# Performance work log

Measured on AMD Instinct MI355X. Metric: run time of the kernel, lower is better.

Reference implementation:

```python
import jax, jax.numpy as jnp
import numpy as np
from jax import lax

T = 0.2  # temperature

def _l2norm(x, axis):
    n = jnp.sqrt(jnp.sum(x * x, axis=axis, keepdims=True))
    return x / jnp.maximum(n, 1e-12)

def setup_inputs() -> dict:
    key = jax.random.key(0)
    k1, k2, k3, k4 = jax.random.split(key, 4)
    B, K, C, H, W, Q = 16, 5, 256, 128, 128, 64
    res1 = jax.random.normal(k1, (B, K, H, W), jnp.float32)
    fea1 = jax.random.normal(k2, (B, C, H, W), jnp.float32)
    gt = jax.random.randint(k3, (B, H, W), 0, K, dtype=jnp.int32)
    # queue buffers, L2-normalized along feature dim (torch normalize(dim=0) on [C,Q])
    queues = _l2norm(jax.random.normal(k4, (K, C, Q), jnp.float32), axis=1)
    return {"res1": res1, "fea1": fea1, "queues": queues, "gt": gt, "label_bs": 8}

def reference(res1, fea1, queues, gt, label_bs):
    B, K, H, W = res1.shape
    C = fea1.shape[1]
    HW = H * W
    # per-sample prediction: gt for labeled samples, argmax of logits otherwise
    pred_arg = jnp.argmax(res1, axis=1).reshape(B, HW)
    pred_gt = gt.reshape(B, HW).astype(pred_arg.dtype)
    labeled = (jnp.arange(B) < label_bs)[:, None]
    pred = jnp.where(labeled, pred_gt, pred_arg)  # [B, HW]

    fea = fea1.reshape(B, C, HW)
    # masked segment-mean per class (vectorized version of the per-unique-label loop)
    onehot = (pred[:, None, :] == jnp.arange(K)[None, :, None]).astype(fea.dtype)  # [B,K,HW]
    counts = onehot.sum(-1)                                    # [B,K]
    sums = jnp.einsum('bkp,bcp->bkc', onehot, fea)             # [B,K,C]
    means = sums / jnp.maximum(counts, 1.0)[..., None]
    keys_all = _l2norm(means, axis=-1)                         # [B,K,C]

    present = counts > 0                                       # [B,K]
    # Faithful replication of the source's off-by-one: keys[list(vals).index(c)]
    # selects the mean of the PREVIOUS present class (vals excludes the smallest
    # present label while keys keeps all unique labels in sorted order).
    idx = jnp.where(present, jnp.arange(K)[None, :], -1)
    cmax = lax.cummax(idx, axis=1)
    prev = jnp.concatenate([jnp.full((B, 1), -1, cmax.dtype), cmax[:, :-1]], axis=1)  # [B,K]
    smallest = jnp.argmax(present, axis=1)                     # first present class
    valid = present & (jnp.arange(K)[None, :] != smallest[:, None]) & (prev >= 0)

    query = jnp.take_along_axis(keys_all, jnp.maximum(prev, 0)[:, :, None], axis=1)  # [B,K,C]

    qd = lax.stop_gradient(queues)  # queues are detached buffers in the original
    sim = jnp.einsum('bkc,jcq->bkjq', query, qd) / T           # [B,K,K,Q]
    l_pos = jnp.einsum('bkc,kcq->bkq', query, qd) / T          # [B,K,Q]
    sumE = jnp.exp(sim).sum(-1)                                # [B,K,K]
    off = 1.0 - jnp.eye(K, dtype=sumE.dtype)
    neg = (sumE * off[None]).sum(-1)                           # [B,K] cross-class negatives
    l_neg = jnp.exp(l_pos) + neg[:, :, None]                   # [B,K,Q]
    log_prob = (l_pos - jnp.log(l_neg)).mean(-1)               # [B,K]

    loss_c = jnp.where(valid, -log_prob, 0.0)
    n_present = present.sum(1)
    denom = n_present - 1  # len(vals)
    per_sample = jnp.where(denom > 0, loss_c.sum(1) / jnp.maximum(denom, 1), 0.0)
    return per_sample.sum() / B
```

## Files before the change

### kernel.cpp

```cpp
#include <hip/hip_runtime.h>
#include <cstddef>

constexpr int B_  = 16;
constexpr int K_  = 5;
constexpr int C_  = 256;
constexpr int HW_ = 128 * 128;
constexpr int Q_  = 64;
constexpr float T_ = 0.2f;

typedef float f4 __attribute__((ext_vector_type(4)));

__global__ __launch_bounds__(256) void pred_kernel(
    const float* __restrict__ res1, const int* __restrict__ gt,
    const int* __restrict__ label_bs, unsigned int* __restrict__ predp,
    int* __restrict__ counts_i)
{
    int idx = blockIdx.x * 256 + threadIdx.x;
    int b  = idx >> 12;
    int p4 = idx & 4095;
    int lb = label_bs[0];
    int k0, k1, k2, k3;
    if (b < lb) {
        int4 g = reinterpret_cast<const int4*>(gt + (size_t)b * HW_)[p4];
        k0 = g.x; k1 = g.y; k2 = g.z; k3 = g.w;
    } else {
        const float4* r = reinterpret_cast<const float4*>(res1 + (size_t)b * K_ * HW_) + p4;
        float4 best = r[0];
        k0 = k1 = k2 = k3 = 0;
        #pragma unroll
        for (int k = 1; k < K_; ++k) {
            float4 v = r[(size_t)k * (HW_ / 4)];
            if (v.x > best.x) { best.x = v.x; k0 = k; }
            if (v.y > best.y) { best.y = v.y; k1 = k; }
            if (v.z > best.z) { best.z = v.z; k2 = k; }
            if (v.w > best.w) { best.w = v.w; k3 = k; }
        }
    }
    predp[idx] = (unsigned)k0 | ((unsigned)k1 << 8) | ((unsigned)k2 << 16) | ((unsigned)k3 << 24);

    int cnt[K_];
    #pragma unroll
    for (int k = 0; k < K_; ++k)
        cnt[k] = (k0 == k) + (k1 == k) + (k2 == k) + (k3 == k);

    int lane = threadIdx.x & 63, wv = threadIdx.x >> 6;
    __shared__ int redc[4][K_];
    #pragma unroll
    for (int k = 0; k < K_; ++k) {
        int v = cnt[k];
        #pragma unroll
        for (int off = 32; off > 0; off >>= 1) v += __shfl_down(v, off);
        if (lane == 0) redc[wv][k] = v;
    }
    __syncthreads();
    if (threadIdx.x < K_)
        atomicAdd(&counts_i[b * K_ + threadIdx.x],
                  redc[0][threadIdx.x] + redc[1][threadIdx.x] +
                  redc[2][threadIdx.x] + redc[3][threadIdx.x]);
}

__global__ __launch_bounds__(256) void segsum_kernel(
    const float* __restrict__ fea, const unsigned int* __restrict__ predp,
    float* __restrict__ sums)
{
    int tid = threadIdx.x;
    int lane = tid & 63, wv = tid >> 6;
    __shared__ float red[4][K_];

    #pragma unroll
    for (int r = 0; r < 2; ++r) {
        int bc = blockIdx.x + r * 2048;
        int b = bc >> 8;
        int c = bc & (C_ - 1);
        const f4* frow = reinterpret_cast<const f4*>(fea + ((size_t)b * C_ + c) * HW_);
        const unsigned int* prow = predp + (size_t)b * (HW_ / 4);

        float acc[K_] = {};
        #pragma unroll 4
        for (int i = tid; i < HW_ / 4; i += 256) {
            f4 v = __builtin_nontemporal_load(frow + i);
            unsigned u = prow[i];
            int k0 = u & 255, k1 = (u >> 8) & 255, k2 = (u >> 16) & 255, k3 = u >> 24;
            #pragma unroll
            for (int k = 0; k < K_; ++k) {
                acc[k] += (k0 == k ? v.x : 0.f)
                        + (k1 == k ? v.y : 0.f)
                        + (k2 == k ? v.z : 0.f)
                        + (k3 == k ? v.w : 0.f);
            }
        }

        #pragma unroll
        for (int k = 0; k < K_; ++k) {
            float v = acc[k];
            #pragma unroll
            for (int off = 32; off > 0; off >>= 1) v += __shfl_down(v, off);
            if (lane == 0) red[wv][k] = v;
        }
        __syncthreads();
        if (tid < K_)
            sums[((size_t)b * K_ + tid) * C_ + c] =
                red[0][tid] + red[1][tid] + red[2][tid] + red[3][tid];
        __syncthreads();
    }
}

__global__ __launch_bounds__(256) void loss_kernel(
    const float* __restrict__ sums, const int* __restrict__ counts_i,
    const float* __restrict__ queues, float* __restrict__ logprob,
    int* __restrict__ flag, float* __restrict__ out)
{
    int bk = blockIdx.x;
    int b = bk / K_;
    int k = bk - b * K_;
    int tid = threadIdx.x, lane = tid & 63, wv = tid >> 6;

    __shared__ float key[C_];
    __shared__ float wred[4];
    __shared__ float sumE_s[K_];
    __shared__ float lpos_s[Q_];
    __shared__ int   last_s;

    int cv[K_];
    #pragma unroll
    for (int j = 0; j < K_; ++j) cv[j] = counts_i[b * K_ + j];
    int prev = -1;
    #pragma unroll
    for (int j = 0; j < K_; ++j)
        if (j < k && cv[j] > 0) prev = j;
    int pk = prev < 0 ? 0 : prev;

    float m = sums[((size_t)b * K_ + pk) * C_ + tid] / fmaxf((float)cv[pk], 1.0f);
    float s = m * m;
    #pragma unroll
    for (int off = 32; off > 0; off >>= 1) s += __shfl_down(s, off);
    if (lane == 0) wred[wv] = s;
    __syncthreads();
    float nrm = sqrtf(wred[0] + wred[1] + wred[2] + wred[3]);
    key[tid] = m / fmaxf(nrm, 1e-12f);
    __syncthreads();

    for (int j = wv; j < K_; j += 4) {
        const float* qj = queues + (size_t)j * C_ * Q_ + lane;
        float acc = 0.f;
        for (int c = 0; c < C_; ++c)
            acc += key[c] * qj[(size_t)c * Q_];
        acc = acc / T_;
        float e = expf(acc);
        float se = e;
        #pragma unroll
        for (int off = 32; off > 0; off >>= 1) se += __shfl_down(se, off);
        if (lane == 0) sumE_s[j] = se;
        if (j == k) lpos_s[lane] = acc;
    }
    __syncthreads();

    if (wv == 0) {
        float neg = 0.f;
        #pragma unroll
        for (int j = 0; j < K_; ++j)
            if (j != k) neg += sumE_s[j];
        float lp = lpos_s[lane];
        float term = lp - logf(expf(lp) + neg);
        #pragma unroll
        for (int off = 32; off > 0; off >>= 1) term += __shfl_down(term, off);
        if (lane == 0) logprob[bk] = term * (1.0f / (float)Q_);
    }
    __syncthreads();

    if (tid == 0) {
        __threadfence();
        last_s = (atomicAdd(flag, 1) == B_ * K_ - 1);
    }
    __syncthreads();
    if (last_s && wv == 0) {
        __threadfence();
        float per = 0.f;
        if (lane < B_) {
            int last = -1, smallest = -1, npres = 0;
            float lsum = 0.f;
            #pragma unroll
            for (int kk = 0; kk < K_; ++kk) {
                bool pres = counts_i[lane * K_ + kk] > 0;
                bool valid = pres && smallest >= 0 && last >= 0;
                if (valid) lsum += -logprob[lane * K_ + kk];
                if (pres && smallest < 0) smallest = kk;
                if (pres) { ++npres; last = kk; }
            }
            int denom = npres - 1;
            per = (denom > 0) ? (lsum / (float)denom) : 0.f;
        }
        #pragma unroll
        for (int off = 32; off > 0; off >>= 1) per += __shfl_down(per, off);
        if (lane == 0) out[0] = per / (float)B_;
    }
}

extern "C" void kernel_launch(void* const* d_in, const int* in_sizes, int n_in,
                              void* d_out, int out_size, void* d_ws, size_t ws_size,
                              hipStream_t stream)
{
    const float* res1     = (const float*)d_in[0];
    const float* fea1     = (const float*)d_in[1];
    const float* queues   = (const float*)d_in[2];
    const int*   gt       = (const int*)d_in[3];
    const int*   label_bs = (const int*)d_in[4];
    float* out = (float*)d_out;

    char* ws = (char*)d_ws;
    unsigned int* predp = (unsigned int*)ws;
    float* sums     = (float*)(ws + (size_t)B_ * (HW_ / 4) * 4);
    int*   counts_i = (int*)(sums + (size_t)B_ * K_ * C_);
    int*   flag     = counts_i + B_ * K_;
    float* logprob  = (float*)(flag + 1);

    hipMemsetAsync(counts_i, 0, (B_ * K_ + 1) * sizeof(int), stream);

    pred_kernel<<<B_ * HW_ / 4 / 256, 256, 0, stream>>>(res1, gt, label_bs, predp, counts_i);
    segsum_kernel<<<2048, 256, 0, stream>>>(fea1, predp, sums);
    loss_kernel<<<B_ * K_, 256, 0, stream>>>(sums, counts_i, queues, logprob, flag, out);
}
```

Measured before the change: 70.15 us.

## Drop memset via per-block counts, one (b,c) row per segsum block

Removes the hipMemsetAsync by having pred_kernel reset the flag and write per-block class counts, which loss_kernel then reduces instead of relying on atomics into a zeroed buffer. segsum now launches 4096 blocks with one channel row each instead of 2048 blocks that each loop over two rows. res1 loads in the argmax become nontemporal. The aim is to save the memset launch and improve load balance, at the cost of a small extra count reduction in the loss kernel and a flag reset that depends on kernel ordering.

```diff
diff --git a/kernel.cpp b/kernel.cpp
--- a/kernel.cpp
+++ b/kernel.cpp
@@ -7,14 +7,18 @@
 constexpr int HW_ = 128 * 128;
 constexpr int Q_  = 64;
 constexpr float T_ = 0.2f;
+constexpr int WPS_ = HW_ / 4;
+constexpr int PB_  = 16;
 
 typedef float f4 __attribute__((ext_vector_type(4)));
 
 __global__ __launch_bounds__(256) void pred_kernel(
     const float* __restrict__ res1, const int* __restrict__ gt,
     const int* __restrict__ label_bs, unsigned int* __restrict__ predp,
-    int* __restrict__ counts_i)
-{
+    int* __restrict__ counts_blk, int* __restrict__ flag)
+{
+    if (blockIdx.x == 0 && threadIdx.x == 0) *flag = 0;
+
     int idx = blockIdx.x * 256 + threadIdx.x;
     int b  = idx >> 12;
     int p4 = idx & 4095;
@@ -24,19 +28,20 @@
         int4 g = reinterpret_cast<const int4*>(gt + (size_t)b * HW_)[p4];
         k0 = g.x; k1 = g.y; k2 = g.z; k3 = g.w;
     } else {
-        const float4* r = reinterpret_cast<const float4*>(res1 + (size_t)b * K_ * HW_) + p4;
-        float4 best = r[0];
+        const f4* r = reinterpret_cast<const f4*>(res1 + (size_t)b * K_ * HW_) + p4;
+        f4 best = __builtin_nontemporal_load(r);
         k0 = k1 = k2 = k3 = 0;
         #pragma unroll
         for (int k = 1; k < K_; ++k) {
-            float4 v = r[(size_t)k * (HW_ / 4)];
+            f4 v = __builtin_nontemporal_load(r + (size_t)k * WPS_);
             if (v.x > best.x) { best.x = v.x; k0 = k; }
             if (v.y > best.y) { best.y = v.y; k1 = k; }
             if (v.z > best.z) { best.z = v.z; k2 = k; }
             if (v.w > best.w) { best.w = v.w; k3 = k; }
         }
     }
-    predp[idx] = (unsigned)k0 | ((unsigned)k1 << 8) | ((unsigned)k2 << 16) | ((unsigned)k3 << 24);
+    predp[idx] = (unsigned)(k0 & 0xFF) | ((unsigned)(k1 & 0xFF) << 8)
+               | ((unsigned)(k2 & 0xFF) << 16) | ((unsigned)(k3 & 0xFF) << 24);
 
     int cnt[K_];
     #pragma unroll
@@ -54,61 +59,56 @@
     }
     __syncthreads();
     if (threadIdx.x < K_)
-        atomicAdd(&counts_i[b * K_ + threadIdx.x],
-                  redc[0][threadIdx.x] + redc[1][threadIdx.x] +
-                  redc[2][threadIdx.x] + redc[3][threadIdx.x]);
+        counts_blk[blockIdx.x * K_ + threadIdx.x] =
+            redc[0][threadIdx.x] + redc[1][threadIdx.x] +
+            redc[2][threadIdx.x] + redc[3][threadIdx.x];
 }
 
 __global__ __launch_bounds__(256) void segsum_kernel(
     const float* __restrict__ fea, const unsigned int* __restrict__ predp,
     float* __restrict__ sums)
 {
+    int bc = blockIdx.x;
+    int b = bc >> 8;
+    int c = bc & (C_ - 1);
     int tid = threadIdx.x;
+    const f4* frow = reinterpret_cast<const f4*>(fea + ((size_t)b * C_ + c) * HW_);
+    const unsigned int* prow = predp + (size_t)b * WPS_;
+
+    float acc[K_] = {};
+    #pragma unroll 4
+    for (int i = tid; i < WPS_; i += 256) {
+        f4 v = __builtin_nontemporal_load(frow + i);
+        unsigned u = prow[i];
+        int k0 = u & 255, k1 = (u >> 8) & 255, k2 = (u >> 16) & 255, k3 = u >> 24;
+        #pragma unroll
+        for (int k = 0; k < K_; ++k) {
+            acc[k] += (k0 == k ? v.x : 0.f)
+                    + (k1 == k ? v.y : 0.f)
+                    + (k2 == k ? v.z : 0.f)
+                    + (k3 == k ? v.w : 0.f);
+        }
+    }
+
+    __shared__ float red[4][K_];
     int lane = tid & 63, wv = tid >> 6;
-    __shared__ float red[4][K_];
-
-    #pragma unroll
-    for (int r = 0; r < 2; ++r) {
-        int bc = blockIdx.x + r * 2048;
-        int b = bc >> 8;
-        int c = bc & (C_ - 1);
-        const f4* frow = reinterpret_cast<const f4*>(fea + ((size_t)b * C_ + c) * HW_);
-        const unsigned int* prow = predp + (size_t)b * (HW_ / 4);
-
-        float acc[K_] = {};
-        #pragma unroll 4
-        for (int i = tid; i < HW_ / 4; i += 256) {
-            f4 v = __builtin_nontemporal_load(frow + i);
-            unsigned u = prow[i];
-            int k0 = u & 255, k1 = (u >> 8) & 255, k2 = (u >> 16) & 255, k3 = u >> 24;
-            #pragma unroll
-            for (int k = 0; k < K_; ++k) {
-                acc[k] += (k0 == k ? v.x : 0.f)
-                        + (k1 == k ? v.y : 0.f)
-                        + (k2 == k ? v.z : 0.f)
-                        + (k3 == k ? v.w : 0.f);
-            }
-        }
-
-        #pragma unroll
-        for (int k = 0; k < K_; ++k) {
-            float v = acc[k];
-            #pragma unroll
-            for (int off = 32; off > 0; off >>= 1) v += __shfl_down(v, off);
-            if (lane == 0) red[wv][k] = v;
-        }
-        __syncthreads();
-        if (tid < K_)
-            sums[((size_t)b * K_ + tid) * C_ + c] =
-                red[0][tid] + red[1][tid] + red[2][tid] + red[3][tid];
-        __syncthreads();
-    }
+    #pragma unroll
+    for (int k = 0; k < K_; ++k) {
+        float v = acc[k];
+        #pragma unroll
+        for (int off = 32; off > 0; off >>= 1) v += __shfl_down(v, off);
+        if (lane == 0) red[wv][k] = v;
+    }
+    __syncthreads();
+    if (tid < K_)
+        sums[((size_t)b * K_ + tid) * C_ + c] =
+            red[0][tid] + red[1][tid] + red[2][tid] + red[3][tid];
 }
 
 __global__ __launch_bounds__(256) void loss_kernel(
-    const float* __restrict__ sums, const int* __restrict__ counts_i,
+    const float* __restrict__ sums, const int* __restrict__ counts_blk,
     const float* __restrict__ queues, float* __restrict__ logprob,
-    int* __restrict__ flag, float* __restrict__ out)
+    int* __restrict__ counts_g, int* __restrict__ flag, float* __restrict__ out)
 {
     int bk = blockIdx.x;
     int b = bk / K_;
@@ -119,18 +119,26 @@
     __shared__ float wred[4];
     __shared__ float sumE_s[K_];
     __shared__ float lpos_s[Q_];
+    __shared__ int   cnt_s[K_];
     __shared__ int   last_s;
 
-    int cv[K_];
-    #pragma unroll
-    for (int j = 0; j < K_; ++j) cv[j] = counts_i[b * K_ + j];
+    if (tid < K_) {
+        int s = 0;
+        #pragma unroll
+        for (int blk = 0; blk < PB_; ++blk)
+            s += counts_blk[(b * PB_ + blk) * K_ + tid];
+        cnt_s[tid] = s;
+        if (k == 0) counts_g[b * K_ + tid] = s;
+    }
+    __syncthreads();
+
     int prev = -1;
     #pragma unroll
     for (int j = 0; j < K_; ++j)
-        if (j < k && cv[j] > 0) prev = j;
+        if (j < k && cnt_s[j] > 0) prev = j;
     int pk = prev < 0 ? 0 : prev;
 
-    float m = sums[((size_t)b * K_ + pk) * C_ + tid] / fmaxf((float)cv[pk], 1.0f);
+    float m = sums[((size_t)b * K_ + pk) * C_ + tid] / fmaxf((float)cnt_s[pk], 1.0f);
     float s = m * m;
     #pragma unroll
     for (int off = 32; off > 0; off >>= 1) s += __shfl_down(s, off);
@@ -181,7 +189,7 @@
             float lsum = 0.f;
             #pragma unroll
             for (int kk = 0; kk < K_; ++kk) {
-                bool pres = counts_i[lane * K_ + kk] > 0;
+                bool pres = counts_g[lane * K_ + kk] > 0;
                 bool valid = pres && smallest >= 0 && last >= 0;
                 if (valid) lsum += -logprob[lane * K_ + kk];
                 if (pres && smallest < 0) smallest = kk;
@@ -209,14 +217,15 @@
 
     char* ws = (char*)d_ws;
     unsigned int* predp = (unsigned int*)ws;
-    float* sums     = (float*)(ws + (size_t)B_ * (HW_ / 4) * 4);
-    int*   counts_i = (int*)(sums + (size_t)B_ * K_ * C_);
-    int*   flag     = counts_i + B_ * K_;
-    float* logprob  = (float*)(flag + 1);
-
-    hipMemsetAsync(counts_i, 0, (B_ * K_ + 1) * sizeof(int), stream);
-
-    pred_kernel<<<B_ * HW_ / 4 / 256, 256, 0, stream>>>(res1, gt, label_bs, predp, counts_i);
-    segsum_kernel<<<2048, 256, 0, stream>>>(fea1, predp, sums);
-    loss_kernel<<<B_ * K_, 256, 0, stream>>>(sums, counts_i, queues, logprob, flag, out);
-}
+    float* sums       = (float*)(ws + (size_t)B_ * WPS_ * 4);
+    int*   counts_blk = (int*)(sums + (size_t)B_ * K_ * C_);
+    int*   counts_g   = counts_blk + B_ * PB_ * K_;
+    int*   flag       = counts_g + B_ * K_;
+    float* logprob    = (float*)(flag + 1);
+
+    pred_kernel<<<B_ * WPS_ / 256, 256, 0, stream>>>(res1, gt, label_bs, predp,
+                                                     counts_blk, flag);
+    segsum_kernel<<<B_ * C_, 256, 0, stream>>>(fea1, predp, sums);
+    loss_kernel<<<B_ * K_, 256, 0, stream>>>(sums, counts_blk, queues, logprob,
+                                             counts_g, flag, out);
+}
```

Result: faster. 64.00 us (-8.8%).
